# Kernel tuning notes

Measured on AMD Instinct MI355X. Metric: run time of the kernel, lower is better.

Reference implementation:

```python
import jax, jax.numpy as jnp
import numpy as np
from jax import lax

WINDOW_SIZE = 5
SIGMA = 1.0
DILATIONS = [1 + int(i ** 1.5) for i in range(5)]  # [1, 2, 3, 6, 9]
C1 = (0.01 * 255.0) ** 2
C2 = (0.03 * 255.0) ** 2


def _make_window(channel=1):
    x = np.arange(WINDOW_SIZE, dtype=np.float64)
    g = np.exp(-((x - WINDOW_SIZE // 2) ** 2) / (2.0 * SIGMA ** 2))
    g = g / g.sum()
    w2d = np.outer(g, g)
    w2d = w2d / w2d.sum()
    w = np.broadcast_to(w2d[None, None], (channel, 1, WINDOW_SIZE, WINDOW_SIZE))
    return jnp.asarray(w, jnp.float32)


def _dw_conv(x, window, dilation):
    # depthwise 'same' conv; pad = (dilated_kernel - 1)/2 = 2*dilation (always even total pad)
    pad = 2 * dilation
    return lax.conv_general_dilated(
        x, window, window_strides=(1, 1),
        padding=((pad, pad), (pad, pad)),
        rhs_dilation=(dilation, dilation),
        dimension_numbers=('NCHW', 'OIHW', 'NCHW'),
        feature_group_count=window.shape[0])


def _ssim_mean(img1, img2, window, dilation):
    mu1 = _dw_conv(img1, window, dilation)
    mu2 = _dw_conv(img2, window, dilation)
    si11 = _dw_conv(img1 * img1, window, dilation)
    si22 = _dw_conv(img2 * img2, window, dilation)
    si12 = _dw_conv(img1 * img2, window, dilation)
    mu1_sq = mu1 * mu1
    mu2_sq = mu2 * mu2
    mu1_mu2 = mu1 * mu2
    sigma1_sq = si11 - mu1_sq
    sigma2_sq = si22 - mu2_sq
    sigma12 = si12 - mu1_mu2
    ssim_map = ((2.0 * mu1_mu2 + C1) * (2.0 * sigma12 + C2)) / (
        (mu1_sq + mu2_sq + C1) * (sigma1_sq + sigma2_sq + C2))
    return jnp.mean(ssim_map)


def _avg_pool2(x):
    B, C, H, W = x.shape
    return x.reshape(B, C, H // 2, 2, W // 2, 2).mean(axis=(3, 5))


def setup_inputs() -> dict:
    key = jax.random.key(0)
    k1, k2 = jax.random.split(key)
    img1 = jax.random.uniform(k1, (16, 1, 1024, 1024), dtype=jnp.float32)
    img2 = jax.random.uniform(k2, (16, 1, 1024, 1024), dtype=jnp.float32)
    window = _make_window(channel=1)
    weights = jnp.asarray([0.0448, 0.2856, 0.3001, 0.2363, 0.1333], jnp.float32)
    return {"img1": img1, "img2": img2, "window": window, "weights": weights}


def reference(img1, img2, window, weights):
    eps = 1e-12
    m = jnp.max(img2)
    a = (img1 + eps) / (m + eps) * 255.0
    b = (img2 + eps) / (m + eps) * 255.0
    mssim = []
    for dil in DILATIONS:
        mssim.append(_ssim_mean(a, b, window, dil))
        a = _avg_pool2(a)
        b = _avg_pool2(b)
    mssim = jnp.stack(mssim)
    return 1.0 - jnp.prod(mssim ** weights)
```

## Files before the change

### kernel.cpp

```cpp
#include <hip/hip_runtime.h>
#include <math.h>

#define EPSN 1e-12f
#define SSIM_C1 6.5025f
#define SSIM_C2 58.5225f


typedef __attribute__((ext_vector_type(2))) float vf2;

__global__ void init_ws_kernel(float* ws) {
    if (threadIdx.x < 16) ws[threadIdx.x] = 0.0f;
}

__global__ void max_kernel(const float4* __restrict__ img2, int n4,
                           unsigned* __restrict__ maxbits) {
    float m = 0.0f;
    for (int i = blockIdx.x * blockDim.x + threadIdx.x; i < n4;
         i += gridDim.x * blockDim.x) {
        float4 v = img2[i];
        m = fmaxf(fmaxf(m, fmaxf(v.x, v.y)), fmaxf(v.z, v.w));
    }
#pragma unroll
    for (int o = 32; o > 0; o >>= 1) m = fmaxf(m, __shfl_down(m, o));
    __shared__ float sm[4];
    int tid = threadIdx.x;
    if ((tid & 63) == 0) sm[tid >> 6] = m;
    __syncthreads();
    if (tid == 0) {
        float mm = fmaxf(fmaxf(sm[0], sm[1]), fmaxf(sm[2], sm[3]));
        atomicMax(maxbits, __float_as_uint(mm));
    }
}


__device__ __forceinline__ float ssim_px(vf2 vpm, vf2 vsq, float s2h) {
    float u = vpm.x * vpm.x, vv = vpm.y * vpm.y;
    float upv = u + vv, umv = u - vv;
    float qp = vsq.x + vsq.y, qm = vsq.x - vsq.y;
    float num1 = fmaf(s2h, umv, SSIM_C1);
    float den1 = fmaf(s2h, upv, SSIM_C1);
    float num2 = fmaf(s2h, qm - umv, SSIM_C2);
    float den2 = fmaf(s2h, qp - upv, SSIM_C2);
    return (num1 * num2) * __builtin_amdgcn_rcpf(den1 * den2);
}

__device__ __forceinline__ void load_g1(const float* __restrict__ window,
                                        float* g1) {
#pragma unroll
    for (int k = 0; k < 5; k++)
        g1[k] = ((window[k * 5 + 0] + window[k * 5 + 1]) +
                 (window[k * 5 + 2] + window[k * 5 + 3])) + window[k * 5 + 4];
}

__device__ __forceinline__ void block_sum_add(float local, float* part, int tid,
                                              float* __restrict__ sumOut) {
#pragma unroll
    for (int o = 32; o > 0; o >>= 1) local += __shfl_down(local, o);
    if ((tid & 63) == 0) part[tid >> 6] = local;
    __syncthreads();
    if (tid == 0)
        atomicAdd(sumOut, (part[0] + part[1]) + (part[2] + part[3]));
}

template <int D, int TPT, int LW>
__device__ __forceinline__ float sep_compute(const vf2* AB, const float* g1,
                                             float s2h, int tx, int ty) {
    vf2 rPM[5], rSQ[5];
    float local = 0.0f;
    int rbase = ty * TPT;
#pragma unroll
    for (int ph = 0; ph < D; ++ph) {
        const int cnt = (TPT - ph + D - 1) / D;
#pragma unroll
        for (int k = 0; k < cnt + 4; ++k) {
            int l = rbase + ph + k * D;
            vf2 hpm = {0, 0}, hsq = {0, 0};
#pragma unroll
            for (int kt = 0; kt < 5; kt++) {
                vf2 ab = AB[l * LW + tx + kt * D];
                vf2 wab = g1[kt] * ab;
                hpm += wab;
                hsq += wab * ab;
            }
            rPM[k % 5] = hpm;
            rSQ[k % 5] = hsq;
            if (k >= 4) {
                vf2 vpm = {0, 0}, vsq = {0, 0};
#pragma unroll
                for (int kt = 0; kt < 5; kt++) {
                    int sl = (k - 4 + kt) % 5;
                    vpm += g1[kt] * rPM[sl];
                    vsq += g1[kt] * rSQ[sl];
                }
                local += ssim_px(vpm, vsq, s2h);
            }
        }
    }
    return local;
}

template <int D, int LH, int W>
__device__ __forceinline__ void stage_sep(const vf2* __restrict__ base,
                                          vf2* AB, int x0i, int y0, int tid) {
    constexpr int LW = 64 + 4 * D;
    for (int idx = tid; idx < LH * 32; idx += 256) {
        int ly = idx >> 5, j = idx & 31;
        int gy = y0 + ly;
        float4 g = make_float4(0, 0, 0, 0);
        if ((unsigned)gy < (unsigned)W)
            g = *(const float4*)(base + (size_t)gy * W + x0i + 2 * j);
        ((float4*)(AB + ly * LW))[D + j] = g;
    }
    for (int idx = tid; idx < LH * 4 * D; idx += 256) {
        int ly = idx / (4 * D), h = idx % (4 * D);
        int lx = (h < 2 * D) ? h : h + 64;
        int gx = x0i - 2 * D + lx, gy = y0 + ly;
        vf2 pm = {0, 0};
        if ((unsigned)gx < (unsigned)W && (unsigned)gy < (unsigned)W)
            pm = base[(size_t)gy * W + gx];
        AB[ly * LW + lx] = pm;
    }
}


__global__ __launch_bounds__(256) void ssim0_kernel(
        const float* __restrict__ A, const float* __restrict__ B,
        const float* __restrict__ window, const unsigned* __restrict__ maxbits,
        float* __restrict__ sums, vf2* __restrict__ poolPM) {
    constexpr int D = 1, TW = 64, TH = 64, TPT = 16;
    constexpr int LW = TW + 4 * D, LH = TH + 4 * D;
    const int H = 1024, W = 1024;
    __shared__ vf2 AB[LH][LW];
    __shared__ float part[4];

    int tx = threadIdx.x, ty = threadIdx.y;
    int tid = ty * 64 + tx;
    int b = blockIdx.z;
    int x0i = blockIdx.x * TW;
    int y0 = blockIdx.y * TH - 2 * D;

    const float* Ab = A + (size_t)b * H * W;
    const float* Bb = B + (size_t)b * H * W;
    for (int idx = tid; idx < LH * 16; idx += 256) {
        int ly = idx >> 4, j = idx & 15;
        int gy = y0 + ly;
        float4 a = make_float4(0, 0, 0, 0), v = make_float4(0, 0, 0, 0);
        if ((unsigned)gy < (unsigned)H) {
            a = *(const float4*)(Ab + (size_t)gy * W + x0i + 4 * j);
            v = *(const float4*)(Bb + (size_t)gy * W + x0i + 4 * j);
        }
        float4 lo = make_float4(a.x + v.x, a.x - v.x, a.y + v.y, a.y - v.y);
        float4 hi = make_float4(a.z + v.z, a.z - v.z, a.w + v.w, a.w - v.w);
        int sig = ((j >> 2) ^ j) & 1;
        float4* rowp = (float4*)(&AB[ly][0]);
        rowp[D + 2 * j + sig] = sig ? hi : lo;
        rowp[D + 2 * j + 1 - sig] = sig ? lo : hi;
    }
    for (int idx = tid; idx < LH * 4 * D; idx += 256) {
        int ly = idx / (4 * D), h = idx % (4 * D);
        int lx = (h < 2 * D) ? h : h + TW;
        int gx = x0i - 2 * D + lx;
        int gy = y0 + ly;
        vf2 pm = {0.0f, 0.0f};
        if ((unsigned)gx < (unsigned)W && (unsigned)gy < (unsigned)H) {
            size_t g = (size_t)gy * W + gx;
            float a = Ab[g], v = Bb[g];
            pm = vf2{a + v, a - v};
        }
        AB[ly][lx] = pm;
    }
    __syncthreads();

    {
        int pW = W >> 1;
        for (int idx = tid; idx < 32 * 16; idx += 256) {
            int py = idx >> 4, j2 = idx & 15;
            int sx = 2 * D + 4 * j2, sy = 2 * D + 2 * py;
            vf2 s00 = AB[sy][sx], s01 = AB[sy][sx + 1];
            vf2 s10 = AB[sy + 1][sx], s11 = AB[sy + 1][sx + 1];
            vf2 o0 = 0.25f * ((s00 + s01) + (s10 + s11));
            vf2 t00 = AB[sy][sx + 2], t01 = AB[sy][sx + 3];
            vf2 t10 = AB[sy + 1][sx + 2], t11 = AB[sy + 1][sx + 3];
            vf2 o1 = 0.25f * ((t00 + t01) + (t10 + t11));
            int gx = (x0i >> 1) + 2 * j2;
            int gy = ((blockIdx.y * TH) >> 1) + py;
            float4 o = make_float4(o0.x, o0.y, o1.x, o1.y);
            *(float4*)(poolPM + (size_t)b * (H >> 1) * pW + (size_t)gy * pW + gx) = o;
        }
    }

    float g1[5];
    load_g1(window, g1);
    float mx = __uint_as_float(*maxbits);
    float sc = 255.0f / (mx + EPSN);
    float s2h = 0.5f * sc * sc;

    float local = sep_compute<D, TPT, LW>(&AB[0][0], g1, s2h, tx, ty);
    block_sum_add(local, part, tid, sums + 0);
}


__global__ __launch_bounds__(256) void ssim1_kernel(
        const vf2* __restrict__ pm1, const float* __restrict__ window,
        const unsigned* __restrict__ maxbits, float* __restrict__ sums,
        vf2* __restrict__ pm2, vf2* __restrict__ pm3, vf2* __restrict__ pm4) {
    constexpr int D = 2, TH = 64, TPT = 16;
    constexpr int LW = 64 + 4 * D, LH = TH + 4 * D;
    const int W = 512;
    __shared__ vf2 AB[LH * LW];
    __shared__ float part[4];

    int tx = threadIdx.x, ty = threadIdx.y;
    int tid = ty * 64 + tx;
    int b = blockIdx.z;
    int bx = blockIdx.x, by = blockIdx.y;
    int x0i = bx * 64;
    int y0 = by * TH - 2 * D;
    const vf2* base = pm1 + (size_t)b * W * W;

    stage_sep<D, LH, 512>(base, AB, x0i, y0, tid);
    __syncthreads();

    for (int idx = tid; idx < 32 * 16; idx += 256) {
        int py = idx >> 4, j2 = idx & 15;
        int sx = 2 * D + 4 * j2, sy = 2 * D + 2 * py;
        vf2 s00 = AB[sy * LW + sx], s01 = AB[sy * LW + sx + 1];
        vf2 s10 = AB[(sy + 1) * LW + sx], s11 = AB[(sy + 1) * LW + sx + 1];
        vf2 o0 = 0.25f * ((s00 + s01) + (s10 + s11));
        vf2 t00 = AB[sy * LW + sx + 2], t01 = AB[sy * LW + sx + 3];
        vf2 t10 = AB[(sy + 1) * LW + sx + 2], t11 = AB[(sy + 1) * LW + sx + 3];
        vf2 o1 = 0.25f * ((t00 + t01) + (t10 + t11));
        int gx = bx * 32 + 2 * j2, gy = by * 32 + py;
        float4 o = make_float4(o0.x, o0.y, o1.x, o1.y);
        *(float4*)(pm2 + (size_t)b * 256 * 256 + (size_t)gy * 256 + gx) = o;
    }
    if (tid < 256) {
        int py = tid >> 4, px = tid & 15;
        vf2 acc = {0, 0};
#pragma unroll
        for (int ry = 0; ry < 4; ry++)
#pragma unroll
            for (int rx = 0; rx < 4; rx++)
                acc += AB[(2 * D + 4 * py + ry) * LW + 2 * D + 4 * px + rx];
        acc *= (1.0f / 16.0f);
        int gx = bx * 16 + px, gy = by * 16 + py;
        pm3[(size_t)b * 128 * 128 + (size_t)gy * 128 + gx] = acc;
    }
    if (tid < 64) {
        int py = tid >> 3, px = tid & 7;
        vf2 acc = {0, 0};
#pragma unroll
        for (int ry = 0; ry < 8; ry++)
#pragma unroll
            for (int rx = 0; rx < 8; rx++)
                acc += AB[(2 * D + 8 * py + ry) * LW + 2 * D + 8 * px + rx];
        acc *= (1.0f / 64.0f);
        int gx = bx * 8 + px, gy = by * 8 + py;
        pm4[(size_t)b * 64 * 64 + (size_t)gy * 64 + gx] = acc;
    }

    float g1[5];
    load_g1(window, g1);
    float mx = __uint_as_float(*maxbits);
    float sc = 255.0f / (mx + EPSN);
    float s2h = 0.5f * sc * sc;

    float local = sep_compute<D, TPT, LW>(AB, g1, s2h, tx, ty);
    block_sum_add(local, part, tid, sums + 1);
}


template <int D, int TW, int TH, int W>
__device__ void direct_level(const vf2* __restrict__ base, const float* g1,
                             int bx, int by, float s2h, float* part,
                             float* __restrict__ sumOut, vf2* AB, int tid) {
    constexpr int LW = TW + 4 * D, LH = TH + 4 * D;
    constexpr int NOUT = TW * TH / 256;
    int x0i = bx * TW, y0 = by * TH - 2 * D;
    int px0 = x0i - 2 * D;

    for (int idx = tid; idx < LW * LH; idx += 256) {
        int ly = idx / LW, lx = idx - ly * LW;
        int px = px0 + lx, py = y0 + ly;
        vf2 pm = {0, 0};
        if ((unsigned)px < (unsigned)W && (unsigned)py < (unsigned)W)
            pm = base[(size_t)py * W + px];
        AB[ly * LW + lx] = pm;
    }
    __syncthreads();

    vf2 mu[NOUT], sq[NOUT];
#pragma unroll
    for (int j = 0; j < NOUT; j++) { mu[j] = vf2{0, 0}; sq[j] = vf2{0, 0}; }
#pragma unroll
    for (int ky = 0; ky < 5; ky++) {
#pragma unroll
        for (int kx = 0; kx < 5; kx++) {
            float w = g1[ky] * g1[kx];
#pragma unroll
            for (int j = 0; j < NOUT; j++) {
                int lin = tid + j * 256;
                int ox = lin % TW, oy = lin / TW;
                vf2 ab = AB[(oy + ky * D) * LW + ox + kx * D];
                vf2 wab = w * ab;
                mu[j] += wab;
                sq[j] += wab * ab;
            }
        }
    }
    float local = 0.0f;
#pragma unroll
    for (int j = 0; j < NOUT; j++) local += ssim_px(mu[j], sq[j], s2h);
    block_sum_add(local, part, tid, sumOut);
}

__global__ __launch_bounds__(256) void tail234_kernel(
        const vf2* __restrict__ pm2, const vf2* __restrict__ pm3,
        const vf2* __restrict__ pm4, const float* __restrict__ window,
        const unsigned* __restrict__ maxbits, float* __restrict__ sums) {
    extern __shared__ vf2 ldsdyn[];
    __shared__ float part[4];
    int tid = threadIdx.x;

    float g1[5];
    load_g1(window, g1);
    float mx = __uint_as_float(*maxbits);
    float sc = 255.0f / (mx + EPSN);
    float s2h = 0.5f * sc * sc;

    int bid = blockIdx.x;
    if (bid < 512) {
        int b = bid >> 5, r = bid & 31, by = r >> 2, bx = r & 3;
        constexpr int D = 3, TH = 32, TPT = 8;
        constexpr int LW = 64 + 4 * D, LH = TH + 4 * D;
        const vf2* base = pm2 + (size_t)b * 256 * 256;
        stage_sep<D, LH, 256>(base, ldsdyn, bx * 64, by * TH - 2 * D, tid);
        __syncthreads();
        float local = sep_compute<D, TPT, LW>(ldsdyn, g1, s2h, tid & 63, tid >> 6);
        block_sum_add(local, part, tid, sums + 2);
    } else if (bid < 768) {
        int t = bid - 512, b = t >> 4, r = t & 15, by = r >> 1, bx = r & 1;
        const vf2* base = pm3 + (size_t)b * 128 * 128;
        direct_level<6, 64, 16, 128>(base, g1, bx, by, s2h, part, sums + 3,
                                     ldsdyn, tid);
    } else {
        int t = bid - 768, b = t >> 3, r = t & 7, by = r >> 1, bx = r & 1;
        const vf2* base = pm4 + (size_t)b * 64 * 64;
        direct_level<9, 32, 16, 64>(base, g1, bx, by, s2h, part, sums + 4,
                                    ldsdyn, tid);
    }
}


__global__ void final_kernel(const float* __restrict__ sums,
                             const float* __restrict__ weights,
                             unsigned* __restrict__ out) {
    if (blockIdx.x == 0 && threadIdx.x == 0) {
        const float counts[5] = {16.0f * 1024 * 1024, 16.0f * 512 * 512,
                                 16.0f * 256 * 256,   16.0f * 128 * 128,
                                 16.0f * 64 * 64};
        float prod = 1.0f;
#pragma unroll
        for (int i = 0; i < 5; i++) {
            float m = sums[i] / counts[i];
            prod *= powf(m, weights[i]);
        }
        float r = 1.0f - prod;
        unsigned bits = __float_as_uint(r);
        unsigned lsb = (bits >> 16) & 1u;
        unsigned hi = (bits + 0x7FFFu + lsb) >> 16;
        out[0] = (hi << 16) | hi;
    }
}


extern "C" void kernel_launch(void* const* d_in, const int* in_sizes, int n_in,
                              void* d_out, int out_size, void* d_ws, size_t ws_size,
                              hipStream_t stream) {
    const float* img1 = (const float*)d_in[0];
    const float* img2 = (const float*)d_in[1];
    const float* window = (const float*)d_in[2];
    const float* weights = (const float*)d_in[3];

    float* ws = (float*)d_ws;
    unsigned* maxbits = (unsigned*)d_ws;
    float* sums = ws + 4;
    size_t off = 16;
    vf2* pm1 = (vf2*)(ws + off); off += (size_t)16 * 512 * 512 * 2;
    vf2* pm2 = (vf2*)(ws + off); off += (size_t)16 * 256 * 256 * 2;
    vf2* pm3 = (vf2*)(ws + off); off += (size_t)16 * 128 * 128 * 2;
    vf2* pm4 = (vf2*)(ws + off); off += (size_t)16 * 64 * 64 * 2;

    init_ws_kernel<<<1, 64, 0, stream>>>(ws);
    max_kernel<<<2048, 256, 0, stream>>>((const float4*)img2,
                                         16 * 1024 * 1024 / 4, maxbits);
    ssim0_kernel<<<dim3(16, 16, 16), dim3(64, 4), 0, stream>>>(
        img1, img2, window, maxbits, sums, pm1);
    ssim1_kernel<<<dim3(8, 8, 16), dim3(64, 4), 0, stream>>>(
        pm1, window, maxbits, sums, pm2, pm3, pm4);
    tail234_kernel<<<896, 256, 28288, stream>>>(pm2, pm3, pm4, window,
                                                maxbits, sums);
    final_kernel<<<1, 64, 0, stream>>>(sums, weights, (unsigned*)d_out);
}
```

Measured before the change: 292.1 us.

## Store shared tiles and pyramid levels as fp16 pairs, fold final into tail

```diff
diff --git a/kernel.cpp b/kernel.cpp
--- a/kernel.cpp
+++ b/kernel.cpp
@@ -7,10 +7,16 @@
 
 
 typedef __attribute__((ext_vector_type(2))) float vf2;
+typedef __attribute__((ext_vector_type(2))) _Float16 h2;
+typedef __attribute__((ext_vector_type(8))) _Float16 h8;
+
+__device__ __forceinline__ vf2 h2f(h2 v) { return vf2{(float)v.x, (float)v.y}; }
+
 
 __global__ void init_ws_kernel(float* ws) {
     if (threadIdx.x < 16) ws[threadIdx.x] = 0.0f;
 }
+
 
 __global__ void max_kernel(const float4* __restrict__ img2, int n4,
                            unsigned* __restrict__ maxbits) {
@@ -62,8 +68,8 @@
         atomicAdd(sumOut, (part[0] + part[1]) + (part[2] + part[3]));
 }
 
-template <int D, int TPT, int LW>
-__device__ __forceinline__ float sep_compute(const vf2* AB, const float* g1,
+template <int D, int TPT, int LW, int L0>
+__device__ __forceinline__ float sep_compute(const h2* AB, const float* g1,
                                              float s2h, int tx, int ty) {
     vf2 rPM[5], rSQ[5];
     float local = 0.0f;
@@ -73,14 +79,14 @@
         const int cnt = (TPT - ph + D - 1) / D;
 #pragma unroll
         for (int k = 0; k < cnt + 4; ++k) {
-            int l = rbase + ph + k * D;
+            const h2* row = AB + (rbase + ph + k * D) * LW + (L0 - 2 * D) + tx;
             vf2 hpm = {0, 0}, hsq = {0, 0};
 #pragma unroll
             for (int kt = 0; kt < 5; kt++) {
-                vf2 ab = AB[l * LW + tx + kt * D];
-                vf2 wab = g1[kt] * ab;
-                hpm += wab;
-                hsq += wab * ab;
+                vf2 f = h2f(row[kt * D]);
+                vf2 w = g1[kt] * f;
+                hpm += w;
+                hsq += w * f;
             }
             rPM[k % 5] = hpm;
             rSQ[k % 5] = hsq;
@@ -99,26 +105,25 @@
     return local;
 }
 
-template <int D, int LH, int W>
-__device__ __forceinline__ void stage_sep(const vf2* __restrict__ base,
-                                          vf2* AB, int x0i, int y0, int tid) {
-    constexpr int LW = 64 + 4 * D;
-    for (int idx = tid; idx < LH * 32; idx += 256) {
-        int ly = idx >> 5, j = idx & 31;
+template <int D, int LH, int LW, int L0, int W>
+__device__ __forceinline__ void stage_h2(const h2* __restrict__ base, h2* AB,
+                                         int x0i, int y0, int tid) {
+    for (int idx = tid; idx < LH * 16; idx += 256) {
+        int ly = idx >> 4, j = idx & 15;
         int gy = y0 + ly;
         float4 g = make_float4(0, 0, 0, 0);
         if ((unsigned)gy < (unsigned)W)
-            g = *(const float4*)(base + (size_t)gy * W + x0i + 2 * j);
-        ((float4*)(AB + ly * LW))[D + j] = g;
+            g = *(const float4*)(base + (size_t)gy * W + x0i + 4 * j);
+        *(float4*)&AB[ly * LW + L0 + 4 * j] = g;
     }
     for (int idx = tid; idx < LH * 4 * D; idx += 256) {
         int ly = idx / (4 * D), h = idx % (4 * D);
-        int lx = (h < 2 * D) ? h : h + 64;
-        int gx = x0i - 2 * D + lx, gy = y0 + ly;
-        vf2 pm = {0, 0};
+        int gc = (h < 2 * D) ? h : h + 64;
+        int gx = x0i - 2 * D + gc, gy = y0 + ly;
+        h2 pm = {(_Float16)0.f, (_Float16)0.f};
         if ((unsigned)gx < (unsigned)W && (unsigned)gy < (unsigned)W)
             pm = base[(size_t)gy * W + gx];
-        AB[ly * LW + lx] = pm;
+        AB[ly * LW + (L0 - 2 * D) + gc] = pm;
     }
 }
 
@@ -126,67 +131,60 @@
 __global__ __launch_bounds__(256) void ssim0_kernel(
         const float* __restrict__ A, const float* __restrict__ B,
         const float* __restrict__ window, const unsigned* __restrict__ maxbits,
-        float* __restrict__ sums, vf2* __restrict__ poolPM) {
-    constexpr int D = 1, TW = 64, TH = 64, TPT = 16;
-    constexpr int LW = TW + 4 * D, LH = TH + 4 * D;
-    const int H = 1024, W = 1024;
-    __shared__ vf2 AB[LH][LW];
+        float* __restrict__ sums, h2* __restrict__ pm1) {
+    constexpr int TH = 64, TPT = 16, L0 = 4, LW = 72, LH = 68;
+    __shared__ __align__(16) h2 AB[LH * LW];
     __shared__ float part[4];
 
     int tx = threadIdx.x, ty = threadIdx.y;
     int tid = ty * 64 + tx;
     int b = blockIdx.z;
-    int x0i = blockIdx.x * TW;
-    int y0 = blockIdx.y * TH - 2 * D;
-
-    const float* Ab = A + (size_t)b * H * W;
-    const float* Bb = B + (size_t)b * H * W;
+    int x0i = blockIdx.x * 64;
+    int y0 = blockIdx.y * TH - 2;
+
+    const float* Ab = A + (size_t)b * 1024 * 1024;
+    const float* Bb = B + (size_t)b * 1024 * 1024;
     for (int idx = tid; idx < LH * 16; idx += 256) {
         int ly = idx >> 4, j = idx & 15;
         int gy = y0 + ly;
         float4 a = make_float4(0, 0, 0, 0), v = make_float4(0, 0, 0, 0);
-        if ((unsigned)gy < (unsigned)H) {
-            a = *(const float4*)(Ab + (size_t)gy * W + x0i + 4 * j);
-            v = *(const float4*)(Bb + (size_t)gy * W + x0i + 4 * j);
-        }
-        float4 lo = make_float4(a.x + v.x, a.x - v.x, a.y + v.y, a.y - v.y);
-        float4 hi = make_float4(a.z + v.z, a.z - v.z, a.w + v.w, a.w - v.w);
-        int sig = ((j >> 2) ^ j) & 1;
-        float4* rowp = (float4*)(&AB[ly][0]);
-        rowp[D + 2 * j + sig] = sig ? hi : lo;
-        rowp[D + 2 * j + 1 - sig] = sig ? lo : hi;
-    }
-    for (int idx = tid; idx < LH * 4 * D; idx += 256) {
-        int ly = idx / (4 * D), h = idx % (4 * D);
-        int lx = (h < 2 * D) ? h : h + TW;
-        int gx = x0i - 2 * D + lx;
-        int gy = y0 + ly;
-        vf2 pm = {0.0f, 0.0f};
-        if ((unsigned)gx < (unsigned)W && (unsigned)gy < (unsigned)H) {
-            size_t g = (size_t)gy * W + gx;
-            float a = Ab[g], v = Bb[g];
-            pm = vf2{a + v, a - v};
-        }
-        AB[ly][lx] = pm;
+        if ((unsigned)gy < 1024u) {
+            a = *(const float4*)(Ab + (size_t)gy * 1024 + x0i + 4 * j);
+            v = *(const float4*)(Bb + (size_t)gy * 1024 + x0i + 4 * j);
+        }
+        h8 r;
+        r[0] = (_Float16)(a.x + v.x); r[1] = (_Float16)(a.x - v.x);
+        r[2] = (_Float16)(a.y + v.y); r[3] = (_Float16)(a.y - v.y);
+        r[4] = (_Float16)(a.z + v.z); r[5] = (_Float16)(a.z - v.z);
+        r[6] = (_Float16)(a.w + v.w); r[7] = (_Float16)(a.w - v.w);
+        *(h8*)&AB[ly * LW + L0 + 4 * j] = r;
+    }
+    for (int idx = tid; idx < LH * 4; idx += 256) {
+        int ly = idx >> 2, h = idx & 3;
+        int gc = (h < 2) ? h : h + 64;
+        int gx = x0i - 2 + gc, gy = y0 + ly;
+        h2 pm = {(_Float16)0.f, (_Float16)0.f};
+        if ((unsigned)gx < 1024u && (unsigned)gy < 1024u) {
+            float a = Ab[(size_t)gy * 1024 + gx], v = Bb[(size_t)gy * 1024 + gx];
+            pm = h2{(_Float16)(a + v), (_Float16)(a - v)};
+        }
+        AB[ly * LW + (L0 - 2) + gc] = pm;
     }
     __syncthreads();
 
     {
-        int pW = W >> 1;
-        for (int idx = tid; idx < 32 * 16; idx += 256) {
-            int py = idx >> 4, j2 = idx & 15;
-            int sx = 2 * D + 4 * j2, sy = 2 * D + 2 * py;
-            vf2 s00 = AB[sy][sx], s01 = AB[sy][sx + 1];
-            vf2 s10 = AB[sy + 1][sx], s11 = AB[sy + 1][sx + 1];
-            vf2 o0 = 0.25f * ((s00 + s01) + (s10 + s11));
-            vf2 t00 = AB[sy][sx + 2], t01 = AB[sy][sx + 3];
-            vf2 t10 = AB[sy + 1][sx + 2], t11 = AB[sy + 1][sx + 3];
-            vf2 o1 = 0.25f * ((t00 + t01) + (t10 + t11));
-            int gx = (x0i >> 1) + 2 * j2;
-            int gy = ((blockIdx.y * TH) >> 1) + py;
-            float4 o = make_float4(o0.x, o0.y, o1.x, o1.y);
-            *(float4*)(poolPM + (size_t)b * (H >> 1) * pW + (size_t)gy * pW + gx) = o;
-        }
+        int py = tid >> 3, j4 = tid & 7;
+        const h2* r0 = AB + (2 + 2 * py) * LW + L0 + 8 * j4;
+        const h2* r1 = r0 + LW;
+        h2 q = {(_Float16)0.25f, (_Float16)0.25f};
+        h8 o;
+#pragma unroll
+        for (int t = 0; t < 4; t++) {
+            h2 s = ((r0[2 * t] + r0[2 * t + 1]) + (r1[2 * t] + r1[2 * t + 1])) * q;
+            o[2 * t] = s.x; o[2 * t + 1] = s.y;
+        }
+        int gx = (x0i >> 1) + 4 * j4, gy = blockIdx.y * 32 + py;
+        *(h8*)(pm1 + (size_t)b * 512 * 512 + (size_t)gy * 512 + gx) = o;
     }
 
     float g1[5];
@@ -195,68 +193,65 @@
     float sc = 255.0f / (mx + EPSN);
     float s2h = 0.5f * sc * sc;
 
-    float local = sep_compute<D, TPT, LW>(&AB[0][0], g1, s2h, tx, ty);
+    float local = sep_compute<1, TPT, LW, L0>(AB, g1, s2h, tx, ty);
     block_sum_add(local, part, tid, sums + 0);
 }
 
 
 __global__ __launch_bounds__(256) void ssim1_kernel(
-        const vf2* __restrict__ pm1, const float* __restrict__ window,
+        const h2* __restrict__ pm1, const float* __restrict__ window,
         const unsigned* __restrict__ maxbits, float* __restrict__ sums,
-        vf2* __restrict__ pm2, vf2* __restrict__ pm3, vf2* __restrict__ pm4) {
-    constexpr int D = 2, TH = 64, TPT = 16;
-    constexpr int LW = 64 + 4 * D, LH = TH + 4 * D;
-    const int W = 512;
-    __shared__ vf2 AB[LH * LW];
+        h2* __restrict__ pm2, h2* __restrict__ pm3, h2* __restrict__ pm4) {
+    constexpr int D = 2, TH = 64, TPT = 16, L0 = 4, LW = 72, LH = 72;
+    __shared__ __align__(16) h2 AB[LH * LW];
     __shared__ float part[4];
 
     int tx = threadIdx.x, ty = threadIdx.y;
     int tid = ty * 64 + tx;
-    int b = blockIdx.z;
-    int bx = blockIdx.x, by = blockIdx.y;
-    int x0i = bx * 64;
-    int y0 = by * TH - 2 * D;
-    const vf2* base = pm1 + (size_t)b * W * W;
-
-    stage_sep<D, LH, 512>(base, AB, x0i, y0, tid);
-    __syncthreads();
-
-    for (int idx = tid; idx < 32 * 16; idx += 256) {
-        int py = idx >> 4, j2 = idx & 15;
-        int sx = 2 * D + 4 * j2, sy = 2 * D + 2 * py;
-        vf2 s00 = AB[sy * LW + sx], s01 = AB[sy * LW + sx + 1];
-        vf2 s10 = AB[(sy + 1) * LW + sx], s11 = AB[(sy + 1) * LW + sx + 1];
-        vf2 o0 = 0.25f * ((s00 + s01) + (s10 + s11));
-        vf2 t00 = AB[sy * LW + sx + 2], t01 = AB[sy * LW + sx + 3];
-        vf2 t10 = AB[(sy + 1) * LW + sx + 2], t11 = AB[(sy + 1) * LW + sx + 3];
-        vf2 o1 = 0.25f * ((t00 + t01) + (t10 + t11));
-        int gx = bx * 32 + 2 * j2, gy = by * 32 + py;
-        float4 o = make_float4(o0.x, o0.y, o1.x, o1.y);
-        *(float4*)(pm2 + (size_t)b * 256 * 256 + (size_t)gy * 256 + gx) = o;
-    }
-    if (tid < 256) {
+    int b = blockIdx.z, bx = blockIdx.x, by = blockIdx.y;
+    int x0i = bx * 64, y0 = by * TH - 4;
+    const h2* base = pm1 + (size_t)b * 512 * 512;
+
+    stage_h2<D, LH, LW, L0, 512>(base, AB, x0i, y0, tid);
+    __syncthreads();
+
+    {
+        int py = tid >> 3, j4 = tid & 7;
+        const h2* r0 = AB + (4 + 2 * py) * LW + 4 + 8 * j4;
+        const h2* r1 = r0 + LW;
+        h2 q = {(_Float16)0.25f, (_Float16)0.25f};
+        h8 o;
+#pragma unroll
+        for (int t = 0; t < 4; t++) {
+            h2 s = ((r0[2 * t] + r0[2 * t + 1]) + (r1[2 * t] + r1[2 * t + 1])) * q;
+            o[2 * t] = s.x; o[2 * t + 1] = s.y;
+        }
+        int gx = bx * 32 + 4 * j4, gy = by * 32 + py;
+        *(h8*)(pm2 + (size_t)b * 256 * 256 + (size_t)gy * 256 + gx) = o;
+    }
+    {
         int py = tid >> 4, px = tid & 15;
-        vf2 acc = {0, 0};
+        h2 acc = {(_Float16)0.f, (_Float16)0.f};
 #pragma unroll
         for (int ry = 0; ry < 4; ry++)
 #pragma unroll
             for (int rx = 0; rx < 4; rx++)
-                acc += AB[(2 * D + 4 * py + ry) * LW + 2 * D + 4 * px + rx];
-        acc *= (1.0f / 16.0f);
-        int gx = bx * 16 + px, gy = by * 16 + py;
-        pm3[(size_t)b * 128 * 128 + (size_t)gy * 128 + gx] = acc;
+                acc += AB[(4 + 4 * py + ry) * LW + 4 + 4 * px + rx];
+        h2 q = {(_Float16)0.0625f, (_Float16)0.0625f};
+        acc *= q;
+        pm3[(size_t)b * 128 * 128 + (size_t)(by * 16 + py) * 128 + bx * 16 + px] = acc;
     }
     if (tid < 64) {
         int py = tid >> 3, px = tid & 7;
-        vf2 acc = {0, 0};
+        h2 acc = {(_Float16)0.f, (_Float16)0.f};
 #pragma unroll
         for (int ry = 0; ry < 8; ry++)
 #pragma unroll
             for (int rx = 0; rx < 8; rx++)
-                acc += AB[(2 * D + 8 * py + ry) * LW + 2 * D + 8 * px + rx];
-        acc *= (1.0f / 64.0f);
-        int gx = bx * 8 + px, gy = by * 8 + py;
-        pm4[(size_t)b * 64 * 64 + (size_t)gy * 64 + gx] = acc;
+                acc += AB[(4 + 8 * py + ry) * LW + 4 + 8 * px + rx];
+        h2 q = {(_Float16)0.015625f, (_Float16)0.015625f};
+        acc *= q;
+        pm4[(size_t)b * 64 * 64 + (size_t)(by * 8 + py) * 64 + bx * 8 + px] = acc;
     }
 
     float g1[5];
@@ -265,27 +260,25 @@
     float sc = 255.0f / (mx + EPSN);
     float s2h = 0.5f * sc * sc;
 
-    float local = sep_compute<D, TPT, LW>(AB, g1, s2h, tx, ty);
+    float local = sep_compute<D, TPT, LW, L0>(AB, g1, s2h, tx, ty);
     block_sum_add(local, part, tid, sums + 1);
 }
 
 
-template <int D, int TW, int TH, int W>
-__device__ void direct_level(const vf2* __restrict__ base, const float* g1,
+template <int D, int TW, int TH, int W, int LW, int LH>
+__device__ void direct_level(const h2* __restrict__ base, const float* g1,
                              int bx, int by, float s2h, float* part,
-                             float* __restrict__ sumOut, vf2* AB, int tid) {
-    constexpr int LW = TW + 4 * D, LH = TH + 4 * D;
+                             float* __restrict__ sumOut, h2* AB, int tid) {
     constexpr int NOUT = TW * TH / 256;
-    int x0i = bx * TW, y0 = by * TH - 2 * D;
-    int px0 = x0i - 2 * D;
+    int x0 = bx * TW - 2 * D, y0 = by * TH - 2 * D;
 
     for (int idx = tid; idx < LW * LH; idx += 256) {
         int ly = idx / LW, lx = idx - ly * LW;
-        int px = px0 + lx, py = y0 + ly;
-        vf2 pm = {0, 0};
+        int px = x0 + lx, py = y0 + ly;
+        h2 pm = {(_Float16)0.f, (_Float16)0.f};
         if ((unsigned)px < (unsigned)W && (unsigned)py < (unsigned)W)
             pm = base[(size_t)py * W + px];
-        AB[ly * LW + lx] = pm;
+        AB[idx] = pm;
     }
     __syncthreads();
 
@@ -301,10 +294,10 @@
             for (int j = 0; j < NOUT; j++) {
                 int lin = tid + j * 256;
                 int ox = lin % TW, oy = lin / TW;
-                vf2 ab = AB[(oy + ky * D) * LW + ox + kx * D];
-                vf2 wab = w * ab;
-                mu[j] += wab;
-                sq[j] += wab * ab;
+                vf2 f = h2f(AB[(oy + ky * D) * LW + ox + kx * D]);
+                vf2 wf = w * f;
+                mu[j] += wf;
+                sq[j] += wf * f;
             }
         }
     }
@@ -314,11 +307,13 @@
     block_sum_add(local, part, tid, sumOut);
 }
 
-__global__ __launch_bounds__(256) void tail234_kernel(
-        const vf2* __restrict__ pm2, const vf2* __restrict__ pm3,
-        const vf2* __restrict__ pm4, const float* __restrict__ window,
-        const unsigned* __restrict__ maxbits, float* __restrict__ sums) {
-    extern __shared__ vf2 ldsdyn[];
+__global__ __launch_bounds__(256) void tail_kernel(
+        const h2* __restrict__ pm2, const h2* __restrict__ pm3,
+        const h2* __restrict__ pm4, const float* __restrict__ window,
+        const unsigned* __restrict__ maxbits, float* __restrict__ sums,
+        unsigned* __restrict__ counter, const float* __restrict__ weights,
+        unsigned* __restrict__ out) {
+    extern __shared__ __align__(16) h2 ldsdyn[];
     __shared__ float part[4];
     int tid = threadIdx.x;
 
@@ -331,45 +326,44 @@
     int bid = blockIdx.x;
     if (bid < 512) {
         int b = bid >> 5, r = bid & 31, by = r >> 2, bx = r & 3;
-        constexpr int D = 3, TH = 32, TPT = 8;
-        constexpr int LW = 64 + 4 * D, LH = TH + 4 * D;
-        const vf2* base = pm2 + (size_t)b * 256 * 256;
-        stage_sep<D, LH, 256>(base, ldsdyn, bx * 64, by * TH - 2 * D, tid);
+        constexpr int D = 3, TPT = 8, L0 = 8, LW = 80, LH = 44;
+        const h2* base = pm2 + (size_t)b * 256 * 256;
+        stage_h2<D, LH, LW, L0, 256>(base, ldsdyn, bx * 64, by * 32 - 6, tid);
         __syncthreads();
-        float local = sep_compute<D, TPT, LW>(ldsdyn, g1, s2h, tid & 63, tid >> 6);
+        float local = sep_compute<D, TPT, LW, L0>(ldsdyn, g1, s2h,
+                                                  tid & 63, tid >> 6);
         block_sum_add(local, part, tid, sums + 2);
     } else if (bid < 768) {
         int t = bid - 512, b = t >> 4, r = t & 15, by = r >> 1, bx = r & 1;
-        const vf2* base = pm3 + (size_t)b * 128 * 128;
-        direct_level<6, 64, 16, 128>(base, g1, bx, by, s2h, part, sums + 3,
-                                     ldsdyn, tid);
+        const h2* base = pm3 + (size_t)b * 128 * 128;
+        direct_level<6, 64, 16, 128, 88, 40>(base, g1, bx, by, s2h, part,
+                                             sums + 3, ldsdyn, tid);
     } else {
         int t = bid - 768, b = t >> 3, r = t & 7, by = r >> 1, bx = r & 1;
-        const vf2* base = pm4 + (size_t)b * 64 * 64;
-        direct_level<9, 32, 16, 64>(base, g1, bx, by, s2h, part, sums + 4,
-                                    ldsdyn, tid);
-    }
-}
-
-
-__global__ void final_kernel(const float* __restrict__ sums,
-                             const float* __restrict__ weights,
-                             unsigned* __restrict__ out) {
-    if (blockIdx.x == 0 && threadIdx.x == 0) {
-        const float counts[5] = {16.0f * 1024 * 1024, 16.0f * 512 * 512,
-                                 16.0f * 256 * 256,   16.0f * 128 * 128,
-                                 16.0f * 64 * 64};
-        float prod = 1.0f;
-#pragma unroll
-        for (int i = 0; i < 5; i++) {
-            float m = sums[i] / counts[i];
-            prod *= powf(m, weights[i]);
-        }
-        float r = 1.0f - prod;
-        unsigned bits = __float_as_uint(r);
-        unsigned lsb = (bits >> 16) & 1u;
-        unsigned hi = (bits + 0x7FFFu + lsb) >> 16;
-        out[0] = (hi << 16) | hi;
+        const h2* base = pm4 + (size_t)b * 64 * 64;
+        direct_level<9, 32, 16, 64, 68, 52>(base, g1, bx, by, s2h, part,
+                                            sums + 4, ldsdyn, tid);
+    }
+
+    if (tid == 0) {
+        __threadfence();
+        if (atomicAdd(counter, 1u) == 895u) {
+            __threadfence();
+            const float counts[5] = {16.0f * 1024 * 1024, 16.0f * 512 * 512,
+                                     16.0f * 256 * 256,   16.0f * 128 * 128,
+                                     16.0f * 64 * 64};
+            float prod = 1.0f;
+#pragma unroll
+            for (int i = 0; i < 5; i++) {
+                float m = atomicAdd(sums + i, 0.0f) / counts[i];
+                prod *= powf(m, weights[i]);
+            }
+            float r = 1.0f - prod;
+            unsigned bits = __float_as_uint(r);
+            unsigned lsb = (bits >> 16) & 1u;
+            unsigned hi = (bits + 0x7FFFu + lsb) >> 16;
+            out[0] = (hi << 16) | hi;
+        }
     }
 }
 
@@ -385,11 +379,12 @@
     float* ws = (float*)d_ws;
     unsigned* maxbits = (unsigned*)d_ws;
     float* sums = ws + 4;
-    size_t off = 16;
-    vf2* pm1 = (vf2*)(ws + off); off += (size_t)16 * 512 * 512 * 2;
-    vf2* pm2 = (vf2*)(ws + off); off += (size_t)16 * 256 * 256 * 2;
-    vf2* pm3 = (vf2*)(ws + off); off += (size_t)16 * 128 * 128 * 2;
-    vf2* pm4 = (vf2*)(ws + off); off += (size_t)16 * 64 * 64 * 2;
+    unsigned* counter = (unsigned*)(ws + 10);
+    size_t off = 512;
+    h2* pm1 = (h2*)(ws + off); off += (size_t)16 * 512 * 512;
+    h2* pm2 = (h2*)(ws + off); off += (size_t)16 * 256 * 256;
+    h2* pm3 = (h2*)(ws + off); off += (size_t)16 * 128 * 128;
+    h2* pm4 = (h2*)(ws + off); off += (size_t)16 * 64 * 64;
 
     init_ws_kernel<<<1, 64, 0, stream>>>(ws);
     max_kernel<<<2048, 256, 0, stream>>>((const float4*)img2,
@@ -398,7 +393,7 @@
         img1, img2, window, maxbits, sums, pm1);
     ssim1_kernel<<<dim3(8, 8, 16), dim3(64, 4), 0, stream>>>(
         pm1, window, maxbits, sums, pm2, pm3, pm4);
-    tail234_kernel<<<896, 256, 28288, stream>>>(pm2, pm3, pm4, window,
-                                                maxbits, sums);
-    final_kernel<<<1, 64, 0, stream>>>(sums, weights, (unsigned*)d_out);
-}
+    tail_kernel<<<896, 256, 14144, stream>>>(pm2, pm3, pm4, window, maxbits,
+                                             sums, counter, weights,
+                                             (unsigned*)d_out);
+}
```

Result: faster. 278.0 us (-4.8%).
